# Optimization experiments

Hardware: AMD Instinct MI355X
Metric: run time of the kernel (lower is better)

Reference implementation:

```python
import jax, jax.numpy as jnp
import numpy as np
from jax import lax

DEPTH = 2
PATCH_SIZE = 16
PATCH_SIZE_FINAL = PATCH_SIZE // (2 ** DEPTH)  # 4
NUM_CHANNELS = 3
NUM_PATCHES = 196
NUM_PATCHES_FINAL = NUM_PATCHES * (4 ** DEPTH)  # 3136
EMB_DIM = NUM_CHANNELS * PATCH_SIZE_FINAL ** 2  # 48


def patchify(X, p):
    # X: [B, C, H, W] -> [B, (H//p)*(W//p), C, p, p], patches in row-major order
    B, C, H, W = X.shape
    eh, ew = H // p, W // p
    x = X.reshape(B, C, eh, p, ew, p)
    x = x.transpose(0, 2, 4, 1, 3, 5)  # [B, eh, ew, C, p, p]
    return x.reshape(B, eh * ew, C, p, p)


def unpatchify(x):
    # x: [B, n, C, p, p] with n = e*e -> [B, 1, C, e*p, e*p]
    B, n, C, p, _ = x.shape
    e = int(np.sqrt(n))
    img = x.reshape(B, e, e, C, p, p).transpose(0, 3, 1, 4, 2, 5).reshape(B, C, e * p, e * p)
    return img[:, None]  # [B, 1, C, H, W]


def conv_same(X, W, b):
    # NCHW conv with 3x3 kernel, 'same' padding
    y = lax.conv_general_dilated(X, W, window_strides=(1, 1), padding='SAME',
                                 dimension_numbers=('NCHW', 'OIHW', 'NCHW'))
    return y + b[None, :, None, None]


def setup_inputs() -> dict:
    key = jax.random.key(0)
    k1, k2, k3, k4 = jax.random.split(key, 4)
    return {
        'X': jax.random.normal(k1, (128, 3, 224, 224), dtype=jnp.float32),
        'conv_w': jax.random.normal(k2, (3, 3, 3, 3), dtype=jnp.float32) * 0.1,
        'conv_b': jax.random.normal(k3, (3,), dtype=jnp.float32) * 0.1,
        'pos_emb': jax.random.normal(k4, (NUM_PATCHES_FINAL, EMB_DIM), dtype=jnp.float32),
    }


def reference(X, conv_w, conv_b, pos_emb):
    B = X.shape[0]
    X = conv_same(X, conv_w, conv_b)
    # patch at fine granularity and add learned position embeddings
    pat = patchify(X, PATCH_SIZE_FINAL)                      # [B, 3136, 3, 4, 4]
    flat = pat.reshape(B, NUM_PATCHES_FINAL, EMB_DIM) + pos_emb[None]
    # unflatten + unpatch back to full image
    enc = flat.reshape(B, NUM_PATCHES_FINAL, NUM_CHANNELS, PATCH_SIZE_FINAL, PATCH_SIZE_FINAL)
    img = unpatchify(enc)                                    # [B, 1, 3, 224, 224]
    # re-patch at coarse granularity (patch() squeezes the singleton dim)
    out = patchify(img[:, 0], PATCH_SIZE)                    # [B, 196, 3, 16, 16]
    return out.reshape(B, NUM_PATCHES, NUM_CHANNELS * PATCH_SIZE ** 2)
```

## Files before the change

### kernel.cpp

```cpp
#include <hip/hip_runtime.h>

#define HW 224
#define CHW (HW*HW)

__global__ __launch_bounds__(256) void patch_conv_kernel(
    const float* __restrict__ X,
    const float* __restrict__ Wt,
    const float* __restrict__ Bv,
    const float* __restrict__ P,
    float* __restrict__ out)
{
    const int tid  = threadIdx.x;
    const int lane = tid & 63;
    const int wv   = tid >> 6;
    const int b    = blockIdx.y;
    const int y0   = blockIdx.x * 8 + wv * 2;
    const int x0   = lane * 4;
    const bool act = (x0 < HW);

    float w[81];
    #pragma unroll
    for (int i = 0; i < 81; ++i) w[i] = Wt[i];

    const float* Xb = X + (size_t)b * (3 * CHW);

    float4 v[3][4];
    #pragma unroll
    for (int ci = 0; ci < 3; ++ci) {
        #pragma unroll
        for (int rj = 0; rj < 4; ++rj) {
            const int ry = y0 - 1 + rj;
            float4 t = make_float4(0.f, 0.f, 0.f, 0.f);
            if ((unsigned)ry < HW && act)
                t = *(const float4*)(Xb + ci * CHW + ry * HW + x0);
            v[ci][rj] = t;
        }
    }

    const int nf   = (y0 >> 2) * 56 + lane;
    const int sub0 = (y0 & 3) * 4;
    float4 pr[2][3];
    #pragma unroll
    for (int rr = 0; rr < 2; ++rr) {
        #pragma unroll
        for (int co = 0; co < 3; ++co) {
            float4 t = make_float4(0.f, 0.f, 0.f, 0.f);
            if (act)
                t = *(const float4*)(P + nf * 48 + co * 16 + sub0 + rr * 4);
            pr[rr][co] = t;
        }
    }

    float win[3][4][6];
    #pragma unroll
    for (int ci = 0; ci < 3; ++ci) {
        #pragma unroll
        for (int rj = 0; rj < 4; ++rj) {
            float lf = __shfl_up(v[ci][rj].w, 1);
            float rt = __shfl_down(v[ci][rj].x, 1);
            if (lane == 0) lf = 0.f;
            if (x0 + 4 >= HW) rt = 0.f;
            win[ci][rj][0] = lf;
            win[ci][rj][1] = v[ci][rj].x; win[ci][rj][2] = v[ci][rj].y;
            win[ci][rj][3] = v[ci][rj].z; win[ci][rj][4] = v[ci][rj].w;
            win[ci][rj][5] = rt;
        }
    }

    if (!act) return;

    float acc[2][3][4];
    #pragma unroll
    for (int rr = 0; rr < 2; ++rr) {
        #pragma unroll
        for (int co = 0; co < 3; ++co) {
            const float bb = Bv[co];
            acc[rr][co][0] = bb + pr[rr][co].x;
            acc[rr][co][1] = bb + pr[rr][co].y;
            acc[rr][co][2] = bb + pr[rr][co].z;
            acc[rr][co][3] = bb + pr[rr][co].w;
        }
    }

    #pragma unroll
    for (int ci = 0; ci < 3; ++ci) {
        #pragma unroll
        for (int ky = 0; ky < 3; ++ky) {
            const float* r0 = win[ci][ky];
            const float* r1 = win[ci][ky + 1];
            #pragma unroll
            for (int co = 0; co < 3; ++co) {
                const float w0 = w[((co * 3 + ci) * 3 + ky) * 3 + 0];
                const float w1 = w[((co * 3 + ci) * 3 + ky) * 3 + 1];
                const float w2 = w[((co * 3 + ci) * 3 + ky) * 3 + 2];
                #pragma unroll
                for (int j = 0; j < 4; ++j) {
                    acc[0][co][j] += w0 * r0[j] + w1 * r0[j + 1] + w2 * r0[j + 2];
                    acc[1][co][j] += w0 * r1[j] + w1 * r1[j + 1] + w2 * r1[j + 2];
                }
            }
        }
    }

    const int nc = (y0 >> 4) * 14 + (x0 >> 4);
    float* opb = out + (size_t)b * (196 * 768) + nc * 768 + (x0 & 15);
    #pragma unroll
    for (int rr = 0; rr < 2; ++rr) {
        float* op = opb + ((y0 + rr) & 15) * 16;
        #pragma unroll
        for (int co = 0; co < 3; ++co)
            *(float4*)(op + co * 256) =
                make_float4(acc[rr][co][0], acc[rr][co][1],
                            acc[rr][co][2], acc[rr][co][3]);
    }
}

extern "C" void kernel_launch(void* const* d_in, const int* in_sizes, int n_in,
                              void* d_out, int out_size, void* d_ws, size_t ws_size,
                              hipStream_t stream) {
    const float* X  = (const float*)d_in[0];
    const float* Wt = (const float*)d_in[1];
    const float* Bv = (const float*)d_in[2];
    const float* P  = (const float*)d_in[3];
    float* out = (float*)d_out;

    dim3 grid(28, 128);
    patch_conv_kernel<<<grid, 256, 0, stream>>>(X, Wt, Bv, P, out);
}
```

Before: 39.37 us.

## Make each wave compute eight rows with a rolling halo window and prefetch

Each wave now loops over four 2-row steps, covering eight output rows. It keeps a rolling 4-row register window per channel and prefetches the next two input rows during each step. This cuts the halo re-read ratio from 2x to about 1.25x, and the blocks shrink to 128 threads with half as many blocks. The cost is less parallelism: about 3.5k waves instead of 14k, with longer serial work per wave. Bias and position terms are now added at store time.

```diff
diff --git a/kernel.cpp b/kernel.cpp
--- a/kernel.cpp
+++ b/kernel.cpp
@@ -3,7 +3,7 @@
 #define HW 224
 #define CHW (HW*HW)
 
-__global__ __launch_bounds__(256) void patch_conv_kernel(
+__global__ __launch_bounds__(128) void patch_conv_kernel(
     const float* __restrict__ X,
     const float* __restrict__ Wt,
     const float* __restrict__ Bv,
@@ -14,15 +14,17 @@
     const int lane = tid & 63;
     const int wv   = tid >> 6;
     const int b    = blockIdx.y;
-    const int y0   = blockIdx.x * 8 + wv * 2;
+    const int y0   = blockIdx.x * 16 + wv * 8;
     const int x0   = lane * 4;
     const bool act = (x0 < HW);
 
     float w[81];
     #pragma unroll
     for (int i = 0; i < 81; ++i) w[i] = Wt[i];
+    const float bias[3] = { Bv[0], Bv[1], Bv[2] };
 
     const float* Xb = X + (size_t)b * (3 * CHW);
+    float* ob = out + (size_t)b * (196 * 768);
 
     float4 v[3][4];
     #pragma unroll
@@ -37,81 +39,108 @@
         }
     }
 
-    const int nf   = (y0 >> 2) * 56 + lane;
-    const int sub0 = (y0 & 3) * 4;
-    float4 pr[2][3];
     #pragma unroll
-    for (int rr = 0; rr < 2; ++rr) {
-        #pragma unroll
-        for (int co = 0; co < 3; ++co) {
-            float4 t = make_float4(0.f, 0.f, 0.f, 0.f);
-            if (act)
-                t = *(const float4*)(P + nf * 48 + co * 16 + sub0 + rr * 4);
-            pr[rr][co] = t;
-        }
-    }
+    for (int k = 0; k < 4; ++k) {
+        const int y = y0 + 2 * k;
 
-    float win[3][4][6];
-    #pragma unroll
-    for (int ci = 0; ci < 3; ++ci) {
-        #pragma unroll
-        for (int rj = 0; rj < 4; ++rj) {
-            float lf = __shfl_up(v[ci][rj].w, 1);
-            float rt = __shfl_down(v[ci][rj].x, 1);
-            if (lane == 0) lf = 0.f;
-            if (x0 + 4 >= HW) rt = 0.f;
-            win[ci][rj][0] = lf;
-            win[ci][rj][1] = v[ci][rj].x; win[ci][rj][2] = v[ci][rj].y;
-            win[ci][rj][3] = v[ci][rj].z; win[ci][rj][4] = v[ci][rj].w;
-            win[ci][rj][5] = rt;
-        }
-    }
-
-    if (!act) return;
-
-    float acc[2][3][4];
-    #pragma unroll
-    for (int rr = 0; rr < 2; ++rr) {
-        #pragma unroll
-        for (int co = 0; co < 3; ++co) {
-            const float bb = Bv[co];
-            acc[rr][co][0] = bb + pr[rr][co].x;
-            acc[rr][co][1] = bb + pr[rr][co].y;
-            acc[rr][co][2] = bb + pr[rr][co].z;
-            acc[rr][co][3] = bb + pr[rr][co].w;
-        }
-    }
-
-    #pragma unroll
-    for (int ci = 0; ci < 3; ++ci) {
-        #pragma unroll
-        for (int ky = 0; ky < 3; ++ky) {
-            const float* r0 = win[ci][ky];
-            const float* r1 = win[ci][ky + 1];
+        float4 nv[3][2];
+        if (k < 3) {
             #pragma unroll
-            for (int co = 0; co < 3; ++co) {
-                const float w0 = w[((co * 3 + ci) * 3 + ky) * 3 + 0];
-                const float w1 = w[((co * 3 + ci) * 3 + ky) * 3 + 1];
-                const float w2 = w[((co * 3 + ci) * 3 + ky) * 3 + 2];
+            for (int ci = 0; ci < 3; ++ci) {
                 #pragma unroll
-                for (int j = 0; j < 4; ++j) {
-                    acc[0][co][j] += w0 * r0[j] + w1 * r0[j + 1] + w2 * r0[j + 2];
-                    acc[1][co][j] += w0 * r1[j] + w1 * r1[j + 1] + w2 * r1[j + 2];
+                for (int rj = 0; rj < 2; ++rj) {
+                    const int ry = y + 3 + rj;
+                    float4 t = make_float4(0.f, 0.f, 0.f, 0.f);
+                    if ((unsigned)ry < HW && act)
+                        t = *(const float4*)(Xb + ci * CHW + ry * HW + x0);
+                    nv[ci][rj] = t;
                 }
             }
         }
-    }
 
-    const int nc = (y0 >> 4) * 14 + (x0 >> 4);
-    float* opb = out + (size_t)b * (196 * 768) + nc * 768 + (x0 & 15);
-    #pragma unroll
-    for (int rr = 0; rr < 2; ++rr) {
-        float* op = opb + ((y0 + rr) & 15) * 16;
+        const int nf   = (y >> 2) * 56 + lane;
+        const int sub0 = (y & 3) * 4;
+        float4 pr[2][3];
         #pragma unroll
-        for (int co = 0; co < 3; ++co)
-            *(float4*)(op + co * 256) =
-                make_float4(acc[rr][co][0], acc[rr][co][1],
-                            acc[rr][co][2], acc[rr][co][3]);
+        for (int rr = 0; rr < 2; ++rr) {
+            #pragma unroll
+            for (int co = 0; co < 3; ++co) {
+                float4 t = make_float4(0.f, 0.f, 0.f, 0.f);
+                if (act)
+                    t = *(const float4*)(P + nf * 48 + co * 16 + sub0 + rr * 4);
+                pr[rr][co] = t;
+            }
+        }
+
+        float win[3][4][6];
+        #pragma unroll
+        for (int ci = 0; ci < 3; ++ci) {
+            #pragma unroll
+            for (int rj = 0; rj < 4; ++rj) {
+                float lf = __shfl_up(v[ci][rj].w, 1);
+                float rt = __shfl_down(v[ci][rj].x, 1);
+                if (lane == 0) lf = 0.f;
+                if (x0 + 4 >= HW) rt = 0.f;
+                win[ci][rj][0] = lf;
+                win[ci][rj][1] = v[ci][rj].x; win[ci][rj][2] = v[ci][rj].y;
+                win[ci][rj][3] = v[ci][rj].z; win[ci][rj][4] = v[ci][rj].w;
+                win[ci][rj][5] = rt;
+            }
+        }
+
+        float acc[2][3][4];
+        #pragma unroll
+        for (int rr = 0; rr < 2; ++rr)
+            #pragma unroll
+            for (int co = 0; co < 3; ++co)
+                #pragma unroll
+                for (int j = 0; j < 4; ++j) acc[rr][co][j] = 0.f;
+
+        #pragma unroll
+        for (int ci = 0; ci < 3; ++ci) {
+            #pragma unroll
+            for (int ky = 0; ky < 3; ++ky) {
+                const float* r0 = win[ci][ky];
+                const float* r1 = win[ci][ky + 1];
+                #pragma unroll
+                for (int co = 0; co < 3; ++co) {
+                    const float w0 = w[((co * 3 + ci) * 3 + ky) * 3 + 0];
+                    const float w1 = w[((co * 3 + ci) * 3 + ky) * 3 + 1];
+                    const float w2 = w[((co * 3 + ci) * 3 + ky) * 3 + 2];
+                    #pragma unroll
+                    for (int j = 0; j < 4; ++j) {
+                        acc[0][co][j] += w0 * r0[j] + w1 * r0[j + 1] + w2 * r0[j + 2];
+                        acc[1][co][j] += w0 * r1[j] + w1 * r1[j + 1] + w2 * r1[j + 2];
+                    }
+                }
+            }
+        }
+
+        if (act) {
+            const int nc = (y >> 4) * 14 + (x0 >> 4);
+            float* opb = ob + nc * 768 + (x0 & 15);
+            #pragma unroll
+            for (int rr = 0; rr < 2; ++rr) {
+                float* op = opb + ((y + rr) & 15) * 16;
+                #pragma unroll
+                for (int co = 0; co < 3; ++co)
+                    *(float4*)(op + co * 256) = make_float4(
+                        acc[rr][co][0] + bias[co] + pr[rr][co].x,
+                        acc[rr][co][1] + bias[co] + pr[rr][co].y,
+                        acc[rr][co][2] + bias[co] + pr[rr][co].z,
+                        acc[rr][co][3] + bias[co] + pr[rr][co].w);
+            }
+        }
+
+        if (k < 3) {
+            #pragma unroll
+            for (int ci = 0; ci < 3; ++ci) {
+                v[ci][0] = v[ci][2];
+                v[ci][1] = v[ci][3];
+                v[ci][2] = nv[ci][0];
+                v[ci][3] = nv[ci][1];
+            }
+        }
     }
 }
 
@@ -124,6 +153,6 @@
     const float* P  = (const float*)d_in[3];
     float* out = (float*)d_out;
 
-    dim3 grid(28, 128);
-    patch_conv_kernel<<<grid, 256, 0, stream>>>(X, Wt, Bv, P, out);
+    dim3 grid(14, 128);
+    patch_conv_kernel<<<grid, 128, 0, stream>>>(X, Wt, Bv, P, out);
 }
```

New measurement: 62.66 us. 1.59x slower.
